# Kernel tuning notes

Hardware: AMD Instinct MI355X
Metric: run time of the kernel (lower is better)

## Reference

```python
import jax, jax.numpy as jnp
import numpy as np

VOCAB, EMB_DIM, HIDDEN, NUM_CLASSES = 100000, 128, 256, 20
B, S = 4096, 200


def setup_inputs() -> dict:
    key = jax.random.key(0)
    k1, k2, k3, k4, k5, k6, k7 = jax.random.split(key, 7)
    x = jax.random.randint(k1, (B, S), 0, VOCAB, dtype=jnp.int64)
    seq_lengths = jnp.maximum(jax.random.randint(k2, (B,), 0, S, dtype=jnp.int64), 1)
    emb = jax.random.normal(k3, (VOCAB, EMB_DIM), dtype=jnp.float32) * 0.02
    emb = emb.at[0].set(0.0)  # padding_idx=0
    W1 = jax.random.normal(k4, (EMB_DIM, HIDDEN), dtype=jnp.float32) * (1.0 / np.sqrt(EMB_DIM))
    b1 = jax.random.normal(k5, (HIDDEN,), dtype=jnp.float32) * 0.01
    W2 = jax.random.normal(k6, (HIDDEN, NUM_CLASSES), dtype=jnp.float32) * (1.0 / np.sqrt(HIDDEN))
    b2 = jax.random.normal(k7, (NUM_CLASSES,), dtype=jnp.float32) * 0.01
    return {"x": x, "seq_lengths": seq_lengths, "emb": emb, "W1": W1, "b1": b1, "W2": W2, "b2": b2}


def reference(x, seq_lengths, emb, W1, b1, W2, b2):
    # Embedding lookup: [B, S, D]
    e = emb[x]
    # Masked mean over first seq_lengths[i] positions (fused, no per-sample loop)
    mask = (jnp.arange(S)[None, :] < seq_lengths[:, None]).astype(e.dtype)  # [B, S]
    pooled = jnp.einsum('bsd,bs->bd', e, mask) / seq_lengths[:, None].astype(e.dtype)
    # MLP (dropout is identity in eval mode)
    hidden = jax.nn.relu(pooled @ W1 + b1)
    return hidden @ W2 + b2
```

## Files before the change

### kernel.cpp

```cpp
#include <hip/hip_runtime.h>

#define B 4096
#define S 200
#define EMB_DIM 128
#define HIDDEN 256
#define NUM_CLASSES 20
#define VOCAB 100000
#define RB 2

typedef __attribute__((ext_vector_type(8))) unsigned short ushort8;

__device__ __forceinline__ unsigned short f2bf(float f) {
    unsigned u = __float_as_uint(f);
    unsigned r = u + 0x7fffu + ((u >> 16) & 1u);
    return (unsigned short)(r >> 16);
}

__global__ __launch_bounds__(256) void convert_kernel(
    const float* __restrict__ emb,
    unsigned short* __restrict__ embh)
{
    const long i = ((long)blockIdx.x * 256 + threadIdx.x) * 8;
    const float4 a = *(const float4*)(emb + i);
    const float4 b = *(const float4*)(emb + i + 4);
    ushort8 o;
    o[0] = f2bf(a.x); o[1] = f2bf(a.y); o[2] = f2bf(a.z); o[3] = f2bf(a.w);
    o[4] = f2bf(b.x); o[5] = f2bf(b.y); o[6] = f2bf(b.z); o[7] = f2bf(b.w);
    *(ushort8*)(embh + i) = o;
}

__global__ __launch_bounds__(256) void fused_kernel(
    const int* __restrict__ x,
    const int* __restrict__ lens,
    const unsigned short* __restrict__ embh,
    const float* __restrict__ W1,
    const float* __restrict__ b1,
    const float* __restrict__ W2,
    const float* __restrict__ b2,
    float* __restrict__ out)
{
    __shared__ int   sidx[RB][256];
    __shared__ float tmp[RB][16][16][8];
    __shared__ float P[RB][EMB_DIM];
    __shared__ float H[RB][HIDDEN];
    __shared__ float part[RB][4][NUM_CLASSES];

    const int t  = threadIdx.x;
    const int b0 = blockIdx.x * RB;

    int Ls[RB];
    #pragma unroll
    for (int r = 0; r < RB; ++r) {
        Ls[r] = lens[b0 + r];
        int v = 0;
        if (t < Ls[r]) v = x[(long)(b0 + r) * S + t];
        sidx[r][t] = v;
    }
    __syncthreads();

    const int g = t >> 4;
    const int d = t & 15;

    const int n0   = (Ls[0] + 63) >> 6;
    const int n1   = (Ls[1] + 63) >> 6;
    const int nMax = n0 > n1 ? n0 : n1;

    float acc[RB][8];
    #pragma unroll
    for (int r = 0; r < RB; ++r)
        #pragma unroll
        for (int f = 0; f < 8; ++f) acc[r][f] = 0.f;

    int cur[RB][4], nxt[RB][4];
    #pragma unroll
    for (int r = 0; r < RB; ++r)
        #pragma unroll
        for (int j = 0; j < 4; ++j) cur[r][j] = sidx[r][g + 16 * j];

    const int dof = d << 3;

    for (int it = 0; it < nMax; ++it) {
        uint4 v[RB][4];
        #pragma unroll
        for (int r = 0; r < RB; ++r)
            #pragma unroll
            for (int j = 0; j < 4; ++j)
                v[r][j] = *(const uint4*)(embh + ((cur[r][j] << 7) + dof));

        const int nb = ((it + 1) & 3) << 6;
        #pragma unroll
        for (int r = 0; r < RB; ++r)
            #pragma unroll
            for (int j = 0; j < 4; ++j) nxt[r][j] = sidx[r][nb + g + 16 * j];

        #pragma unroll
        for (int r = 0; r < RB; ++r)
            #pragma unroll
            for (int j = 0; j < 4; ++j) {
                const unsigned c0 = v[r][j].x, c1 = v[r][j].y;
                const unsigned c2 = v[r][j].z, c3 = v[r][j].w;
                acc[r][0] += __uint_as_float(c0 << 16);
                acc[r][1] += __uint_as_float(c0 & 0xffff0000u);
                acc[r][2] += __uint_as_float(c1 << 16);
                acc[r][3] += __uint_as_float(c1 & 0xffff0000u);
                acc[r][4] += __uint_as_float(c2 << 16);
                acc[r][5] += __uint_as_float(c2 & 0xffff0000u);
                acc[r][6] += __uint_as_float(c3 << 16);
                acc[r][7] += __uint_as_float(c3 & 0xffff0000u);
            }

        #pragma unroll
        for (int r = 0; r < RB; ++r)
            #pragma unroll
            for (int j = 0; j < 4; ++j) cur[r][j] = nxt[r][j];
    }

    #pragma unroll
    for (int r = 0; r < RB; ++r)
        #pragma unroll
        for (int f = 0; f < 8; ++f)
            tmp[r][g][d][f] = acc[r][f];
    __syncthreads();

    {
        const int r   = t >> 7;
        const int dim = t & 127;
        float s = 0.f;
        #pragma unroll
        for (int gg = 0; gg < 16; ++gg) s += tmp[r][gg][dim >> 3][dim & 7];
        P[r][dim] = s / (float)Ls[r];
    }
    __syncthreads();

    {
        float h0a = 0.f, h0b = 0.f, h1a = 0.f, h1b = 0.f;
        for (int k = 0; k < EMB_DIM; k += 2) {
            const float wa = W1[(k)     * HIDDEN + t];
            const float wb = W1[(k + 1) * HIDDEN + t];
            h0a += P[0][k] * wa;  h0b += P[0][k + 1] * wb;
            h1a += P[1][k] * wa;  h1b += P[1][k + 1] * wb;
        }
        const float bb = b1[t];
        H[0][t] = fmaxf(h0a + h0b + bb, 0.f);
        H[1][t] = fmaxf(h1a + h1b + bb, 0.f);
    }
    __syncthreads();

    if (t < RB * 4 * NUM_CLASSES) {
        const int r  = t / (4 * NUM_CLASSES);
        const int u  = t - r * 4 * NUM_CLASSES;
        const int j  = u / NUM_CLASSES;
        const int c  = u - j * NUM_CLASSES;
        const int k0 = j * 64;
        float a = 0.f;
        for (int k = k0; k < k0 + 64; ++k)
            a += H[r][k] * W2[k * NUM_CLASSES + c];
        part[r][j][c] = a;
    }
    __syncthreads();

    if (t < RB * NUM_CLASSES) {
        const int r = t / NUM_CLASSES;
        const int c = t - r * NUM_CLASSES;
        const float a = b2[c] + part[r][0][c] + part[r][1][c]
                              + part[r][2][c] + part[r][3][c];
        out[(long)(b0 + r) * NUM_CLASSES + c] = a;
    }
}

extern "C" void kernel_launch(void* const* d_in, const int* in_sizes, int n_in,
                              void* d_out, int out_size, void* d_ws, size_t ws_size,
                              hipStream_t stream) {
    const int*   x    = (const int*)d_in[0];
    const int*   lens = (const int*)d_in[1];
    const float* emb  = (const float*)d_in[2];
    const float* W1   = (const float*)d_in[3];
    const float* b1   = (const float*)d_in[4];
    const float* W2   = (const float*)d_in[5];
    const float* b2   = (const float*)d_in[6];
    float*       out  = (float*)d_out;

    unsigned short* embh = (unsigned short*)d_ws;

    convert_kernel<<<(VOCAB * EMB_DIM) / (8 * 256), 256, 0, stream>>>(emb, embh);
    fused_kernel<<<B / RB, 256, 0, stream>>>(x, lens, embh, W1, b1, W2, b2, out);
}
```

Before: 125.2 us.

## Process four rows per block with per-row 16-token chunk predication in gather

Doubles rows per block to four and restructures the gather loop into 16-token chunks with two chunks per iteration, skipping loads for chunks beyond each row's length instead of padding to 64-token multiples (which loaded index 0). Reduction of partial sums is done in two halves to reuse the shared tmp buffer, and the MLP loops are widened to four rows so each W1/W2 load is shared across more samples. This cuts wasted gather traffic and amortizes weight reads, at the cost of more loop iterations per block, predication branches, and fewer blocks in flight.

```diff
diff --git a/kernel.cpp b/kernel.cpp
--- a/kernel.cpp
+++ b/kernel.cpp
@@ -6,7 +6,8 @@
 #define HIDDEN 256
 #define NUM_CLASSES 20
 #define VOCAB 100000
-#define RB 2
+#define RB 4
+#define JD 2
 
 typedef __attribute__((ext_vector_type(8))) unsigned short ushort8;
 
@@ -40,10 +41,10 @@
     float* __restrict__ out)
 {
     __shared__ int   sidx[RB][256];
-    __shared__ float tmp[RB][16][16][8];
+    __shared__ float tmp[2][16][16][8];
     __shared__ float P[RB][EMB_DIM];
     __shared__ float H[RB][HIDDEN];
-    __shared__ float part[RB][4][NUM_CLASSES];
+    __shared__ float part[RB][2][NUM_CLASSES];
 
     const int t  = threadIdx.x;
     const int b0 = blockIdx.x * RB;
@@ -58,12 +59,18 @@
     }
     __syncthreads();
 
-    const int g = t >> 4;
-    const int d = t & 15;
-
-    const int n0   = (Ls[0] + 63) >> 6;
-    const int n1   = (Ls[1] + 63) >> 6;
-    const int nMax = n0 > n1 ? n0 : n1;
+    const int g   = t >> 4;
+    const int d   = t & 15;
+    const int dof = d << 3;
+
+    int nC[RB];
+    int nR = 1;
+    #pragma unroll
+    for (int r = 0; r < RB; ++r) {
+        nC[r] = __builtin_amdgcn_readfirstlane((Ls[r] + 15) >> 4);
+        const int rr = (nC[r] + JD - 1) / JD;
+        nR = rr > nR ? rr : nR;
+    }
 
     float acc[RB][8];
     #pragma unroll
@@ -71,100 +78,111 @@
         #pragma unroll
         for (int f = 0; f < 8; ++f) acc[r][f] = 0.f;
 
-    int cur[RB][4], nxt[RB][4];
+    int cur[RB][JD], nxt[RB][JD];
     #pragma unroll
     for (int r = 0; r < RB; ++r)
         #pragma unroll
-        for (int j = 0; j < 4; ++j) cur[r][j] = sidx[r][g + 16 * j];
-
-    const int dof = d << 3;
-
-    for (int it = 0; it < nMax; ++it) {
-        uint4 v[RB][4];
-        #pragma unroll
-        for (int r = 0; r < RB; ++r)
-            #pragma unroll
-            for (int j = 0; j < 4; ++j)
-                v[r][j] = *(const uint4*)(embh + ((cur[r][j] << 7) + dof));
-
-        const int nb = ((it + 1) & 3) << 6;
-        #pragma unroll
-        for (int r = 0; r < RB; ++r)
-            #pragma unroll
-            for (int j = 0; j < 4; ++j) nxt[r][j] = sidx[r][nb + g + 16 * j];
-
-        #pragma unroll
-        for (int r = 0; r < RB; ++r)
-            #pragma unroll
-            for (int j = 0; j < 4; ++j) {
-                const unsigned c0 = v[r][j].x, c1 = v[r][j].y;
-                const unsigned c2 = v[r][j].z, c3 = v[r][j].w;
-                acc[r][0] += __uint_as_float(c0 << 16);
-                acc[r][1] += __uint_as_float(c0 & 0xffff0000u);
-                acc[r][2] += __uint_as_float(c1 << 16);
-                acc[r][3] += __uint_as_float(c1 & 0xffff0000u);
-                acc[r][4] += __uint_as_float(c2 << 16);
-                acc[r][5] += __uint_as_float(c2 & 0xffff0000u);
-                acc[r][6] += __uint_as_float(c3 << 16);
-                acc[r][7] += __uint_as_float(c3 & 0xffff0000u);
-            }
-
-        #pragma unroll
-        for (int r = 0; r < RB; ++r)
-            #pragma unroll
-            for (int j = 0; j < 4; ++j) cur[r][j] = nxt[r][j];
-    }
-
-    #pragma unroll
-    for (int r = 0; r < RB; ++r)
-        #pragma unroll
-        for (int f = 0; f < 8; ++f)
-            tmp[r][g][d][f] = acc[r][f];
+        for (int j = 0; j < JD; ++j) cur[r][j] = sidx[r][(j << 4) + g];
+
+    for (int it = 0; it < nR; ++it) {
+        uint4 v[RB][JD];
+        #pragma unroll
+        for (int r = 0; r < RB; ++r)
+            #pragma unroll
+            for (int j = 0; j < JD; ++j)
+                if (it * JD + j < nC[r])
+                    v[r][j] = *(const uint4*)(embh + ((cur[r][j] << 7) + dof));
+
+        #pragma unroll
+        for (int r = 0; r < RB; ++r)
+            #pragma unroll
+            for (int j = 0; j < JD; ++j)
+                nxt[r][j] = sidx[r][(((it + 1) * JD + j) << 4) + g];
+
+        #pragma unroll
+        for (int r = 0; r < RB; ++r)
+            #pragma unroll
+            for (int j = 0; j < JD; ++j)
+                if (it * JD + j < nC[r]) {
+                    const unsigned c0 = v[r][j].x, c1 = v[r][j].y;
+                    const unsigned c2 = v[r][j].z, c3 = v[r][j].w;
+                    acc[r][0] += __uint_as_float(c0 << 16);
+                    acc[r][1] += __uint_as_float(c0 & 0xffff0000u);
+                    acc[r][2] += __uint_as_float(c1 << 16);
+                    acc[r][3] += __uint_as_float(c1 & 0xffff0000u);
+                    acc[r][4] += __uint_as_float(c2 << 16);
+                    acc[r][5] += __uint_as_float(c2 & 0xffff0000u);
+                    acc[r][6] += __uint_as_float(c3 << 16);
+                    acc[r][7] += __uint_as_float(c3 & 0xffff0000u);
+                }
+
+        #pragma unroll
+        for (int r = 0; r < RB; ++r)
+            #pragma unroll
+            for (int j = 0; j < JD; ++j) cur[r][j] = nxt[r][j];
+    }
+
+    #pragma unroll
+    for (int half = 0; half < 2; ++half) {
+        if (half) __syncthreads();
+        #pragma unroll
+        for (int rr = 0; rr < 2; ++rr)
+            #pragma unroll
+            for (int f = 0; f < 8; ++f)
+                tmp[rr][g][d][f] = acc[half * 2 + rr][f];
+        __syncthreads();
+        {
+            const int rr  = t >> 7;
+            const int dim = t & 127;
+            float s = 0.f;
+            #pragma unroll
+            for (int gg = 0; gg < 16; ++gg) s += tmp[rr][gg][dim >> 3][dim & 7];
+            const float L = rr ? (float)Ls[half * 2 + 1] : (float)Ls[half * 2];
+            P[half * 2 + rr][dim] = s / L;
+        }
+    }
     __syncthreads();
 
     {
-        const int r   = t >> 7;
-        const int dim = t & 127;
-        float s = 0.f;
-        #pragma unroll
-        for (int gg = 0; gg < 16; ++gg) s += tmp[r][gg][dim >> 3][dim & 7];
-        P[r][dim] = s / (float)Ls[r];
-    }
-    __syncthreads();
-
-    {
-        float h0a = 0.f, h0b = 0.f, h1a = 0.f, h1b = 0.f;
+        float hA[RB], hB[RB];
+        #pragma unroll
+        for (int r = 0; r < RB; ++r) { hA[r] = 0.f; hB[r] = 0.f; }
         for (int k = 0; k < EMB_DIM; k += 2) {
             const float wa = W1[(k)     * HIDDEN + t];
             const float wb = W1[(k + 1) * HIDDEN + t];
-            h0a += P[0][k] * wa;  h0b += P[0][k + 1] * wb;
-            h1a += P[1][k] * wa;  h1b += P[1][k + 1] * wb;
+            #pragma unroll
+            for (int r = 0; r < RB; ++r) {
+                hA[r] = fmaf(P[r][k],     wa, hA[r]);
+                hB[r] = fmaf(P[r][k + 1], wb, hB[r]);
+            }
         }
         const float bb = b1[t];
-        H[0][t] = fmaxf(h0a + h0b + bb, 0.f);
-        H[1][t] = fmaxf(h1a + h1b + bb, 0.f);
-    }
-    __syncthreads();
-
-    if (t < RB * 4 * NUM_CLASSES) {
-        const int r  = t / (4 * NUM_CLASSES);
-        const int u  = t - r * 4 * NUM_CLASSES;
+        #pragma unroll
+        for (int r = 0; r < RB; ++r)
+            H[r][t] = fmaxf(hA[r] + hB[r] + bb, 0.f);
+    }
+    __syncthreads();
+
+    if (t < RB * 2 * NUM_CLASSES) {
+        const int r  = t / (2 * NUM_CLASSES);
+        const int u  = t - r * 2 * NUM_CLASSES;
         const int j  = u / NUM_CLASSES;
         const int c  = u - j * NUM_CLASSES;
-        const int k0 = j * 64;
-        float a = 0.f;
-        for (int k = k0; k < k0 + 64; ++k)
-            a += H[r][k] * W2[k * NUM_CLASSES + c];
-        part[r][j][c] = a;
+        const int k0 = j * 128;
+        float a0 = 0.f, a1 = 0.f;
+        for (int k = k0; k < k0 + 128; k += 2) {
+            a0 = fmaf(H[r][k],     W2[(k)     * NUM_CLASSES + c], a0);
+            a1 = fmaf(H[r][k + 1], W2[(k + 1) * NUM_CLASSES + c], a1);
+        }
+        part[r][j][c] = a0 + a1;
     }
     __syncthreads();
 
     if (t < RB * NUM_CLASSES) {
         const int r = t / NUM_CLASSES;
         const int c = t - r * NUM_CLASSES;
-        const float a = b2[c] + part[r][0][c] + part[r][1][c]
-                              + part[r][2][c] + part[r][3][c];
-        out[(long)(b0 + r) * NUM_CLASSES + c] = a;
+        out[(long)(b0 + r) * NUM_CLASSES + c] =
+            b2[c] + part[r][0][c] + part[r][1][c];
     }
 }
 
```

Measured after the change: 127.6 us. Within noise of the previous version (+1.9%).
